# Kernel tuning notes

Measured on AMD Instinct MI355X. Metric: run time of the kernel, lower is better.

The kernel has to match this reference:

```python
import jax, jax.numpy as jnp
import numpy as np

D = 256
N_TOK, N_SRL, N_ENT, T = 50000, 20000, 10000, 50000
E_TS, E_EE, E_ST, E_ET = 300000, 150000, 300000, 150000
SLOPE = 0.01  # F.leaky_relu default negative slope


def _leaky(x):
    return jnp.where(x >= 0, x, SLOPE * x)


def _seg_softmax(e, seg, n):
    # per-destination (segment) softmax over incoming edges, elementwise per feature
    mx = jax.ops.segment_max(e, seg, num_segments=n)
    mx = jnp.where(jnp.isfinite(mx), mx, 0.0)
    ex = jnp.exp(e - mx[seg])
    den = jax.ops.segment_sum(ex, seg, num_segments=n)
    return ex / jnp.maximum(den[seg], 1e-9)


def _gru_cell(x, h, W_ih, W_hh, b_ih, b_hh):
    # PyTorch GRU cell: gates ordered (r, z, n)
    gi = x @ W_ih.T + b_ih
    gh = h @ W_hh.T + b_hh
    ir, iz, in_ = jnp.split(gi, 3, axis=-1)
    hr, hz, hn = jnp.split(gh, 3, axis=-1)
    r = jax.nn.sigmoid(ir + hr)
    z = jax.nn.sigmoid(iz + hz)
    n = jnp.tanh(in_ + r * hn)
    return (1.0 - z) * n + z * h


def _covering_dst(key, E, N):
    # every dst node gets >= 1 edge (matches DGL UDF-reduce update semantics)
    return jax.random.permutation(key, jnp.arange(E, dtype=jnp.int32) % N)


def setup_inputs():
    key = jax.random.key(0)
    ks = jax.random.split(key, 32)
    f32 = jnp.float32
    inp = {
        'feat_tok': jax.random.normal(ks[0], (N_TOK, D), f32),
        'feat_srl': jax.random.normal(ks[1], (N_SRL, D), f32),
        'feat_ent': jax.random.normal(ks[2], (N_ENT, D), f32),
        'bert_token_emb': jax.random.normal(ks[3], (T, D), f32),
        'rel_type': jax.random.uniform(ks[4], (E_EE,), f32),
        'src_ts': jax.random.randint(ks[5], (E_TS,), 0, N_TOK, jnp.int32),
        'dst_ts': _covering_dst(ks[6], E_TS, N_SRL),
        'src_ee': jax.random.randint(ks[7], (E_EE,), 0, N_ENT, jnp.int32),
        'dst_ee': _covering_dst(ks[8], E_EE, N_ENT),
        'src_st': jax.random.randint(ks[9], (E_ST,), 0, N_SRL, jnp.int32),
        'dst_st': _covering_dst(ks[10], E_ST, N_TOK),
        'src_et': jax.random.randint(ks[11], (E_ET,), 0, N_ENT, jnp.int32),
        'dst_et': _covering_dst(ks[12], E_ET, N_TOK),
    }
    x0 = jax.random.randint(ks[13], (E_EE,), 0, T - 64, jnp.int32)
    ln = jax.random.randint(ks[14], (E_EE,), 1, 65, jnp.int32)
    inp['span_idx'] = jnp.stack([x0, x0 + ln], axis=1)
    s = 0.05
    inp['W_node_trans'] = jax.random.normal(ks[15], (D, D), f32) * s
    inp['b_node_trans'] = jnp.zeros((D,), f32)
    inp['W_node_att'] = jax.random.normal(ks[16], (D, 2 * D), f32) * s
    inp['b_node_att'] = jnp.zeros((D,), f32)
    inp['W_rel_trans'] = jax.random.normal(ks[17], (D, 2 * D), f32) * s
    inp['b_rel_trans'] = jnp.zeros((D,), f32)
    inp['W_common'] = jax.random.normal(ks[18], (D, D), f32) * s
    inp['b_common'] = jnp.zeros((D,), f32)
    inp['W_ih'] = jax.random.normal(ks[19], (3 * D, D), f32) * s
    inp['W_hh'] = jax.random.normal(ks[20], (3 * D, D), f32) * s
    inp['b_ih'] = jax.random.normal(ks[21], (3 * D,), f32) * s
    inp['b_hh'] = jax.random.normal(ks[22], (3 * D,), f32) * s
    return inp


def reference(feat_tok, feat_srl, feat_ent, bert_token_emb, rel_type,
              W_node_trans, b_node_trans, W_node_att, b_node_att,
              W_rel_trans, b_rel_trans, W_common, b_common,
              W_ih, W_hh, b_ih, b_hh,
              src_ts, dst_ts, src_ee, dst_ee, span_idx,
              src_st, dst_st, src_et, dst_et):
    # ---- regular edges tok->srl (message_func_regular_node + reduce_func) ----
    us = feat_tok[src_ts] @ W_node_trans.T + b_node_trans          # [E_TS, D]
    ud = feat_srl[dst_ts] @ W_node_trans.T + b_node_trans
    e_ts = _leaky(jnp.concatenate([us, ud], axis=1) @ W_node_att.T + b_node_att)
    alpha_ts = _seg_softmax(e_ts, dst_ts, N_SRL)
    h_srl = jax.ops.segment_sum(alpha_ts * us, dst_ts, num_segments=N_SRL)

    # ---- ent2ent_rel (message_func_rel + reduce_func) ----
    # mean of bert_token_emb[x:y] via prefix sums (vectorized span means)
    P = jnp.concatenate([jnp.zeros((1, D), bert_token_emb.dtype),
                         jnp.cumsum(bert_token_emb, axis=0)], axis=0)  # [T+1, D]
    x, y = span_idx[:, 0], span_idx[:, 1]
    span_mean = (P[y] - P[x]) / (y - x).astype(P.dtype)[:, None]
    rel_emb = rel_type[:, None] * span_mean                         # [E_EE, D]
    src_e = feat_ent[src_ee]
    m_ee = (jnp.concatenate([src_e, rel_emb], axis=1) @ W_rel_trans.T + b_rel_trans)
    m_ee = m_ee @ W_common.T + b_common
    dst_p = feat_ent[dst_ee] @ W_node_trans.T + b_node_trans
    e_ee = _leaky(jnp.concatenate([m_ee, dst_p], axis=1) @ W_node_att.T + b_node_att)
    alpha_ee = _seg_softmax(e_ee, dst_ee, N_ENT)
    h_ent = jax.ops.segment_sum(alpha_ee * m_ee, dst_ee, num_segments=N_ENT)

    # ---- srl2tok / ent2tok: per-edge GRU step then segment-sum on tok ----
    m_st = _gru_cell(h_srl[src_st], feat_tok[dst_st], W_ih, W_hh, b_ih, b_hh)
    h_srl_tok = jax.ops.segment_sum(m_st, dst_st, num_segments=N_TOK)
    m_et = _gru_cell(h_ent[src_et], feat_tok[dst_et], W_ih, W_hh, b_ih, b_hh)
    h_ent_tok = jax.ops.segment_sum(m_et, dst_et, num_segments=N_TOK)

    # ---- final GRU combine: seq (h_ent_tok, feat_tok), hidden h_srl_tok ----
    h1 = _gru_cell(h_ent_tok, h_srl_tok, W_ih, W_hh, b_ih, b_hh)
    h_tok = _gru_cell(feat_tok, h1, W_ih, W_hh, b_ih, b_hh)

    return h_tok, h_srl, h_ent
```

## Files before the change

kernel.cpp:

```cpp
#include <hip/hip_runtime.h>
#include <stdint.h>


typedef unsigned short u16;
typedef __bf16 bf16_t;
typedef bf16_t bf16x8 __attribute__((ext_vector_type(8)));
typedef float f32x4 __attribute__((ext_vector_type(4)));

__device__ __forceinline__ float us2f(u16 h) {
  unsigned int u = ((unsigned int)h) << 16;
  return __builtin_bit_cast(float, u);
}
__device__ __forceinline__ u16 f2us(float f) {
  unsigned int u = __builtin_bit_cast(unsigned int, f);
  u += 0x7FFFu + ((u >> 16) & 1u);
  return (u16)(u >> 16);
}
__device__ __forceinline__ uint4 pack8(float4 a, float4 b) {
  uint4 v;
  v.x = f2us(a.x) | ((unsigned)f2us(a.y) << 16);
  v.y = f2us(a.z) | ((unsigned)f2us(a.w) << 16);
  v.z = f2us(b.x) | ((unsigned)f2us(b.y) << 16);
  v.w = f2us(b.z) | ((unsigned)f2us(b.w) << 16);
  return v;
}
__device__ __forceinline__ void us2f4(ushort4 v, float* o) {
  o[0] = us2f(v.x); o[1] = us2f(v.y); o[2] = us2f(v.z); o[3] = us2f(v.w);
}
__device__ __forceinline__ float sigm(float x) { return 1.f / (1.f + __expf(-x)); }
__device__ __forceinline__ float tanh_f(float x) {
  x = fminf(fmaxf(x, -15.f), 15.f);
  float e = __expf(2.f * x);
  return (e - 1.f) / (e + 1.f);
}

__global__ void fill_sent(float* out, int n, float v) {
  int i = blockIdx.x * 256 + threadIdx.x;
  if (i < n) out[i] = v;
}

__global__ void count_k(const int* __restrict__ dst, int E, int* __restrict__ cnt) {
  int i = blockIdx.x * 256 + threadIdx.x;
  if (i < E) atomicAdd(&cnt[dst[i]], 1);
}

__global__ __launch_bounds__(1024) void scan4_k(int* a0, int n0, int* a1, int n1,
                                                int* a2, int n2, int* a3, int n3) {
  int* a; int n;
  if (blockIdx.x == 0) { a = a0; n = n0; }
  else if (blockIdx.x == 1) { a = a1; n = n1; }
  else if (blockIdx.x == 2) { a = a2; n = n2; }
  else { a = a3; n = n3; }
  __shared__ int swv[16];
  const int t = threadIdx.x, lane = t & 63, wid = t >> 6;
  int carry = 0;
  for (int base = 0; base < n; base += 1024) {
    int r = base + t;
    int v = (r < n) ? a[r] : 0;
    int inc = v;
#pragma unroll
    for (int o = 1; o < 64; o <<= 1) {
      int x = __shfl_up(inc, o, 64);
      if (lane >= o) inc += x;
    }
    if (lane == 63) swv[wid] = inc;
    __syncthreads();
    int wbase = 0, tot = 0;
    for (int w = 0; w < 16; w++) { int s = swv[w]; tot += s; if (w < wid) wbase += s; }
    if (r < n) a[r] = carry + wbase + inc - v;
    carry += tot;
    __syncthreads();
  }
}

__global__ void fill_k(const int* __restrict__ dst, int E, int* __restrict__ off,
                       int* __restrict__ list) {
  int i = blockIdx.x * 256 + threadIdx.x;
  if (i < E) {
    int p = atomicAdd(&off[dst[i]], 1);
    list[p] = i;
  }
}

__global__ __launch_bounds__(256) void cumsum_p1(const float* __restrict__ emb,
                                                 float* __restrict__ bsum) {
  int b = blockIdx.x, t = threadIdx.x;
  int r0 = b * 64, r1 = min(r0 + 64, 50000);
  float acc = 0.f;
  for (int r = r0; r < r1; r++) acc += emb[(size_t)r * 256 + t];
  bsum[(size_t)b * 256 + t] = acc;
}
__global__ __launch_bounds__(256) void cumsum_p2p(float* __restrict__ bsum, int nb) {
  const int d = blockIdx.x;
  const int t = threadIdx.x, lane = t & 63, wid = t >> 6;
  __shared__ float wsum[4];
  float v[4];
  float s = 0.f;
#pragma unroll
  for (int j = 0; j < 4; j++) {
    int b = t * 4 + j;
    v[j] = (b < nb) ? bsum[(size_t)b * 256 + d] : 0.f;
    s += v[j];
  }
  float inc = s;
#pragma unroll
  for (int o = 1; o < 64; o <<= 1) {
    float x = __shfl_up(inc, o, 64);
    if (lane >= o) inc += x;
  }
  if (lane == 63) wsum[wid] = inc;
  __syncthreads();
  float wbase = 0.f;
  for (int w = 0; w < 4; w++) {
    float ws = wsum[w];
    if (w < wid) wbase += ws;
  }
  float excl = wbase + inc - s;
#pragma unroll
  for (int j = 0; j < 4; j++) {
    int b = t * 4 + j;
    if (b < nb) bsum[(size_t)b * 256 + d] = excl;
    excl += v[j];
  }
}
__global__ __launch_bounds__(256) void cumsum_p3(const float* __restrict__ emb,
                                                 const float* __restrict__ bsum,
                                                 float* __restrict__ Pm) {
  int b = blockIdx.x, t = threadIdx.x;
  int r0 = b * 64, r1 = min(r0 + 64, 50000);
  float acc = bsum[(size_t)b * 256 + t];
  if (b == 0) Pm[t] = 0.f;
  for (int r = r0; r < r1; r++) {
    acc += emb[(size_t)r * 256 + t];
    Pm[(size_t)(r + 1) * 256 + t] = acc;
  }
}

__global__ __launch_bounds__(256) void make_B2(const float* __restrict__ Watt,
                                               const float* __restrict__ Wc,
                                               float* __restrict__ B2) {
  int r = blockIdx.x, k = threadIdx.x;
  float s = 0.f;
  for (int n = 0; n < 256; n++) s += Watt[r * 512 + n] * Wc[n * 256 + k];
  B2[r * 256 + k] = s;
}
__global__ void make_bias2(const float* __restrict__ Watt, const float* __restrict__ bc,
                           float* __restrict__ bias2) {
  int r = threadIdx.x;
  float s = 0.f;
  for (int k = 0; k < 256; k++) s += Watt[r * 512 + k] * bc[k];
  bias2[r] = s;
}
__global__ __launch_bounds__(256) void make_WW(const float* __restrict__ Wc,
                                               const float* __restrict__ B2,
                                               const float* __restrict__ Wrel,
                                               float* __restrict__ WW) {
  int r = blockIdx.x, k = threadIdx.x;
  const float* X = (r < 256) ? (Wc + (size_t)r * 256) : (B2 + (size_t)(r - 256) * 256);
  float s = 0.f;
  for (int n = 0; n < 256; n++) s += X[n] * Wrel[(size_t)n * 512 + 256 + k];
  WW[(size_t)r * 256 + k] = s;
}

__global__ __launch_bounds__(256) void conv8(
    const float* s0, u16* d0, int n0, const float* s1, u16* d1, int n1,
    const float* s2, u16* d2, int n2, const float* s3, u16* d3, int n3,
    const float* s4, u16* d4, int n4, const float* s5, u16* d5, int n5,
    const float* s6, u16* d6, int n6, const float* s7, u16* d7, int n7) {
  const float* s; u16* d; int n;
  switch (blockIdx.y) {
    case 0: s = s0; d = d0; n = n0; break;
    case 1: s = s1; d = d1; n = n1; break;
    case 2: s = s2; d = d2; n = n2; break;
    case 3: s = s3; d = d3; n = n3; break;
    case 4: s = s4; d = d4; n = n4; break;
    case 5: s = s5; d = d5; n = n5; break;
    case 6: s = s6; d = d6; n = n6; break;
    default: s = s7; d = d7; n = n7; break;
  }
  int i = (blockIdx.x * 256 + threadIdx.x) * 8;
  if (i < n) {
    float4 a = *(const float4*)(s + i), b = *(const float4*)(s + i + 4);
    *(uint4*)(d + i) = pack8(a, b);
  }
}

template <int AMODE, int ASRC, bool OUTBF>
__global__ __launch_bounds__(256) void gemm_nl(
    const void* __restrict__ Ap, int lda,
    const float* __restrict__ Pm, const int* __restrict__ span,
    const float* __restrict__ rel, const int* __restrict__ lst,
    const int* __restrict__ offarr, const int* __restrict__ srcv,
    const u16* __restrict__ s2tab, int dst0, int dpc,
    const u16* __restrict__ B, int ldb, const float* __restrict__ bias,
    void* __restrict__ Cp, int Cstride, int coff, int M, int NT) {
  constexpr int LDA = 264, LDB = 136;
  __shared__ u16 As[64 * LDA];
  __shared__ u16 Bs[64 * LDB];
  int e_start = 0, eM = M;
  if (AMODE == 2) {
    e_start = dst0 ? offarr[dst0 - 1] : 0;
    int len = offarr[dst0 + dpc - 1] - e_start;
    eM = len < M ? len : M;
  }
  const int m0 = blockIdx.x * 64;
  if (m0 >= eM) return;
  const int nbase = blockIdx.y * NT * 64;
  const int t = threadIdx.x;
  const int wave = t >> 6, lane = t & 63, lrow = lane & 15, quad = lane >> 4;

#pragma unroll
  for (int i = 0; i < 8; i++) {
    int c = t + i * 256;
    int row = c >> 5, col = (c & 31) * 8;
    int gm = m0 + row;
    uint4 va; va.x = va.y = va.z = va.w = 0u;
    if (gm < eM) {
      if (AMODE == 0) {
        if (ASRC == 0) {
          const float* af = (const float*)Ap + (size_t)gm * lda + col;
          va = pack8(*(const float4*)af, *(const float4*)(af + 4));
        } else {
          va = *(const uint4*)((const u16*)Ap + (size_t)gm * lda + col);
        }
      } else {
        int e = lst[e_start + gm];
        int xx = span[2 * e], yy = span[2 * e + 1];
        float sc = rel[e] / (float)(yy - xx);
        const float* py = Pm + (size_t)yy * 256 + col;
        const float* px = Pm + (size_t)xx * 256 + col;
        float4 ya = *(const float4*)py, yb = *(const float4*)(py + 4);
        float4 xa = *(const float4*)px, xb = *(const float4*)(px + 4);
        float4 d0 = {(ya.x - xa.x) * sc, (ya.y - xa.y) * sc,
                     (ya.z - xa.z) * sc, (ya.w - xa.w) * sc};
        float4 d1 = {(yb.x - xb.x) * sc, (yb.y - xb.y) * sc,
                     (yb.z - xb.z) * sc, (yb.w - xb.w) * sc};
        va = pack8(d0, d1);
      }
    }
    *(uint4*)&As[row * LDA + col] = va;
  }

  for (int nt = 0; nt < NT; nt++) {
    const int n0 = nbase + nt * 64;
    f32x4 acc[4] = {{0.f, 0.f, 0.f, 0.f}, {0.f, 0.f, 0.f, 0.f},
                    {0.f, 0.f, 0.f, 0.f}, {0.f, 0.f, 0.f, 0.f}};
    for (int k2 = 0; k2 < 2; k2++) {
      __syncthreads();
#pragma unroll
      for (int i = 0; i < 4; i++) {
        int c = t + i * 256;
        int row = c >> 4, col = (c & 15) * 8;
        uint4 vb = *(const uint4*)(B + (size_t)(n0 + row) * ldb + k2 * 128 + col);
        *(uint4*)&Bs[row * LDB + col] = vb;
      }
      __syncthreads();
      const u16* ab = &As[(wave * 16 + lrow) * LDA + k2 * 128 + quad * 8];
      const u16* bb = &Bs[lrow * LDB + quad * 8];
#pragma unroll
      for (int kk = 0; kk < 128; kk += 32) {
        bf16x8 av = *(const bf16x8*)(ab + kk);
#pragma unroll
        for (int j = 0; j < 4; j++) {
          bf16x8 bv = *(const bf16x8*)(bb + j * 16 * LDB + kk);
          acc[j] = __builtin_amdgcn_mfma_f32_16x16x32_bf16(av, bv, acc[j], 0, 0, 0);
        }
      }
    }
#pragma unroll
    for (int r = 0; r < 4; r++) {
      int m = m0 + wave * 16 + quad * 4 + r;
      if (m < eM) {
        const u16* srow = nullptr;
        if (AMODE == 2) {
          int e = lst[e_start + m];
          srow = s2tab + (size_t)srcv[e] * 512;
        }
#pragma unroll
        for (int j = 0; j < 4; j++) {
          int n = n0 + j * 16 + lrow;
          float v = acc[j][r] + (bias ? bias[n] : 0.f);
          if (AMODE == 2) v += us2f(srow[n]);
          if (OUTBF) ((u16*)Cp)[(size_t)m * Cstride + coff + n] = f2us(v);
          else       ((float*)Cp)[(size_t)m * Cstride + coff + n] = v;
        }
      }
    }
  }
}

__global__ __launch_bounds__(256) void agg_ts2(
    const int* __restrict__ off, const int* __restrict__ list,
    const int* __restrict__ src, const u16* __restrict__ uta,
    const u16* __restrict__ adst, float* __restrict__ out) {
  const int i = blockIdx.x, t = threadIdx.x, lane = t & 63, w = t >> 6;
  const int s0 = i ? off[i - 1] : 0, s1 = off[i];
  const int cnt = s1 - s0;
  __shared__ int sl[64];
  __shared__ float nbuf[4][256], dbuf[4][256];
  if (t < cnt) sl[t] = src[list[s0 + t]];
  __syncthreads();
  const int d4 = lane * 4;
  float ad[4];
  us2f4(*(const ushort4*)&adst[(size_t)i * 256 + d4], ad);
  float num[4] = {0.f, 0.f, 0.f, 0.f}, den[4] = {0.f, 0.f, 0.f, 0.f};
  for (int p = w; p < cnt; p += 4) {
    const u16* row = uta + (size_t)sl[p] * 512;
    float u[4], a[4];
    us2f4(*(const ushort4*)&row[d4], u);
    us2f4(*(const ushort4*)&row[256 + d4], a);
#pragma unroll
    for (int j = 0; j < 4; j++) {
      float v = a[j] + ad[j];
      v = v >= 0.f ? v : 0.01f * v;
      float ex = __expf(v);
      den[j] += ex;
      num[j] += ex * u[j];
    }
  }
#pragma unroll
  for (int j = 0; j < 4; j++) { nbuf[w][d4 + j] = num[j]; dbuf[w][d4 + j] = den[j]; }
  __syncthreads();
  float ns = nbuf[0][t] + nbuf[1][t] + nbuf[2][t] + nbuf[3][t];
  float ds = dbuf[0][t] + dbuf[1][t] + dbuf[2][t] + dbuf[3][t];
  out[(size_t)i * 256 + t] = ns / fmaxf(ds, 1e-9f);
}

__global__ __launch_bounds__(256) void agg_ee2(
    const int* __restrict__ off, const u16* __restrict__ buf,
    const u16* __restrict__ adp, float* __restrict__ out, int dst0) {
  const int i = dst0 + blockIdx.x, t = threadIdx.x, lane = t & 63, w = t >> 6;
  const int e_start = dst0 ? off[dst0 - 1] : 0;
  const int s0 = i ? off[i - 1] : 0, s1 = off[i];
  __shared__ float nbuf[4][256], dbuf[4][256];
  const int d4 = lane * 4;
  float ad[4];
  us2f4(*(const ushort4*)&adp[(size_t)i * 256 + d4], ad);
  float num[4] = {0.f, 0.f, 0.f, 0.f}, den[4] = {0.f, 0.f, 0.f, 0.f};
  for (int p = s0 + w; p < s1; p += 4) {
    const u16* row = buf + (size_t)(p - e_start) * 512;
    float m[4], a[4];
    us2f4(*(const ushort4*)&row[d4], m);
    us2f4(*(const ushort4*)&row[256 + d4], a);
#pragma unroll
    for (int j = 0; j < 4; j++) {
      float v = a[j] + ad[j];
      v = v >= 0.f ? v : 0.01f * v;
      float ex = __expf(v);
      den[j] += ex;
      num[j] += ex * m[j];
    }
  }
#pragma unroll
  for (int j = 0; j < 4; j++) { nbuf[w][d4 + j] = num[j]; dbuf[w][d4 + j] = den[j]; }
  __syncthreads();
  float ns = nbuf[0][t] + nbuf[1][t] + nbuf[2][t] + nbuf[3][t];
  float ds = dbuf[0][t] + dbuf[1][t] + dbuf[2][t] + dbuf[3][t];
  out[(size_t)i * 256 + t] = ns / fmaxf(ds, 1e-9f);
}

__global__ __launch_bounds__(256) void agg_gru2(
    const int* __restrict__ off, const int* __restrict__ list,
    const int* __restrict__ src, const u16* __restrict__ gi,
    const u16* __restrict__ ghc, const float* __restrict__ feat,
    u16* __restrict__ out, int tok0) {
  const int bi = blockIdx.x, i = tok0 + bi;
  const int t = threadIdx.x, lane = t & 63, w = t >> 6;
  const int s0 = i ? off[i - 1] : 0, s1 = off[i];
  const int cnt = s1 - s0;
  __shared__ int sl[32];
  __shared__ float red[4][256];
  if (t < cnt) sl[t] = src[list[s0 + t]];
  __syncthreads();
  const int d4 = lane * 4;
  const size_t b = (size_t)bi * 768;
  float ghr[4], ghz[4], ghn[4], h[4];
  us2f4(*(const ushort4*)&ghc[b + d4], ghr);
  us2f4(*(const ushort4*)&ghc[b + 256 + d4], ghz);
  us2f4(*(const ushort4*)&ghc[b + 512 + d4], ghn);
  { float4 v = *(const float4*)&feat[(size_t)i * 256 + d4];
    h[0] = v.x; h[1] = v.y; h[2] = v.z; h[3] = v.w; }
  float sum[4] = {0.f, 0.f, 0.f, 0.f};
  for (int p = w; p < cnt; p += 4) {
    const u16* g = gi + (size_t)sl[p] * 768;
    float gr[4], gz[4], gn[4];
    us2f4(*(const ushort4*)&g[d4], gr);
    us2f4(*(const ushort4*)&g[256 + d4], gz);
    us2f4(*(const ushort4*)&g[512 + d4], gn);
#pragma unroll
    for (int j = 0; j < 4; j++) {
      float r = sigm(gr[j] + ghr[j]);
      float z = sigm(gz[j] + ghz[j]);
      float n = tanh_f(gn[j] + r * ghn[j]);
      sum[j] += (1.f - z) * n + z * h[j];
    }
  }
#pragma unroll
  for (int j = 0; j < 4; j++) red[w][d4 + j] = sum[j];
  __syncthreads();
  float s = red[0][t] + red[1][t] + red[2][t] + red[3][t];
  out[(size_t)i * 256 + t] = f2us(s);
}

template <bool OUTBF>
__global__ __launch_bounds__(256) void gru_combine2(
    const float* __restrict__ gi, const float* __restrict__ gh,
    const u16* __restrict__ hprev, void* __restrict__ out, int row0) {
  const int t = threadIdx.x, lane = t & 63, w = t >> 6;
  const int li = blockIdx.x * 4 + w;
  const int d4 = lane * 4;
  const size_t g = (size_t)li * 768;
  float4 ir = *(const float4*)&gi[g + d4];
  float4 hr4 = *(const float4*)&gh[g + d4];
  float4 iz = *(const float4*)&gi[g + 256 + d4];
  float4 hz4 = *(const float4*)&gh[g + 256 + d4];
  float4 in4 = *(const float4*)&gi[g + 512 + d4];
  float4 hn4 = *(const float4*)&gh[g + 512 + d4];
  float h[4];
  us2f4(*(const ushort4*)&hprev[(size_t)(row0 + li) * 256 + d4], h);
  float gir[4] = {ir.x, ir.y, ir.z, ir.w}, ghr[4] = {hr4.x, hr4.y, hr4.z, hr4.w};
  float giz[4] = {iz.x, iz.y, iz.z, iz.w}, ghz[4] = {hz4.x, hz4.y, hz4.z, hz4.w};
  float gin[4] = {in4.x, in4.y, in4.z, in4.w}, ghn[4] = {hn4.x, hn4.y, hn4.z, hn4.w};
  float o[4];
#pragma unroll
  for (int j = 0; j < 4; j++) {
    float r = sigm(gir[j] + ghr[j]);
    float z = sigm(giz[j] + ghz[j]);
    float n = tanh_f(gin[j] + r * ghn[j]);
    o[j] = (1.f - z) * n + z * h[j];
  }
  if (OUTBF) {
    ushort4 ov = {f2us(o[0]), f2us(o[1]), f2us(o[2]), f2us(o[3])};
    *(ushort4*)&((u16*)out)[(size_t)(row0 + li) * 256 + d4] = ov;
  } else {
    float4 ov = {o[0], o[1], o[2], o[3]};
    *(float4*)&((float*)out)[(size_t)(row0 + li) * 256 + d4] = ov;
  }
}

extern "C" void kernel_launch(void* const* d_in, const int* in_sizes, int n_in,
                              void* d_out, int out_size, void* d_ws, size_t ws_size,
                              hipStream_t stream) {
  const float* feat_tok = (const float*)d_in[0];
  const float* feat_srl = (const float*)d_in[1];
  const float* feat_ent = (const float*)d_in[2];
  const float* bert     = (const float*)d_in[3];
  const float* rel_type = (const float*)d_in[4];
  const int* src_ts = (const int*)d_in[5];
  const int* dst_ts = (const int*)d_in[6];
  const int* src_ee = (const int*)d_in[7];
  const int* dst_ee = (const int*)d_in[8];
  const int* src_st = (const int*)d_in[9];
  const int* dst_st = (const int*)d_in[10];
  const int* src_et = (const int*)d_in[11];
  const int* dst_et = (const int*)d_in[12];
  const int* span   = (const int*)d_in[13];
  const float* Wn   = (const float*)d_in[14];
  const float* bn   = (const float*)d_in[15];
  const float* Watt = (const float*)d_in[16];
  const float* batt = (const float*)d_in[17];
  const float* Wrel = (const float*)d_in[18];
  const float* brel = (const float*)d_in[19];
  const float* Wc   = (const float*)d_in[20];
  const float* bc   = (const float*)d_in[21];
  const float* Wih  = (const float*)d_in[22];
  const float* Whh  = (const float*)d_in[23];
  const float* bih  = (const float*)d_in[24];
  const float* bhh  = (const float*)d_in[25];

  char* W = (char*)d_ws;
  float* Pm    = (float*)(W + 0);
  u16* uta     = (u16*)(W + 51250240);
  u16* p_srl   = (u16*)(W + 102450240);
  u16* a_dst   = (u16*)(W + 112690240);
  u16* s_ent   = (u16*)(W + 51250240);
  u16* p_ent   = (u16*)(W + 56370240);
  u16* meeatt  = (u16*)(W + 51250240);
  float* WW    = (float*)(W + 138000000);
  float* B2    = (float*)(W + 138600000);
  float* bias2 = (float*)(W + 138900000);
  u16* s2tab   = (u16*)(W + 139000000);
  u16* adp     = (u16*)(W + 149300032);
  float* bsum  = (float*)(W + 155000000);
  u16* gi_srl  = (u16*)(W + 0);
  u16* gi_ent  = (u16*)(W + 30720000);
  u16* ghc     = (u16*)(W + 51250240);
  u16* hst     = (u16*)(W + 115300096);
  u16* het     = (u16*)(W + 140900096);
  float* giA   = (float*)(W + 0);
  float* ghA   = (float*)(W + 38400000);
  u16* h1      = (u16*)(W + 76800000);
  int* ts_off = (int*)(W + 166500096);
  int* ts_lst = (int*)(W + 166580096);
  int* ee_off = (int*)(W + 167780096);
  int* ee_lst = (int*)(W + 167820096);
  int* st_off = (int*)(W + 168420096);
  int* st_lst = (int*)(W + 168620096);
  int* et_off = (int*)(W + 169820096);
  int* et_lst = (int*)(W + 170020096);
  constexpr size_t NEED = 170620096;

  float* out_htok = (float*)d_out;
  float* out_hsrl = (float*)d_out + 12800000;
  float* out_hent = (float*)d_out + 17920000;

  u16* wtb    = (u16*)((char*)d_out + 49000000);
  u16* Wn_b   = wtb;
  u16* Watt_b = wtb + 65536;
  u16* Wrel_b = wtb + 196608;
  u16* Wc_b   = wtb + 327680;
  u16* Wih_b  = wtb + 393216;
  u16* Whh_b  = wtb + 589824;
  u16* WW_b   = wtb + 786432;
  u16* B2_b   = wtb + 917504;

  if (ws_size < NEED) {
    fill_sent<<<(out_size + 255) / 256, 256, 0, stream>>>(
        (float*)d_out, out_size, 1000.f + (float)(ws_size >> 20));
    return;
  }

  hipMemsetAsync(ts_off, 0, 20000 * 4, stream);
  hipMemsetAsync(ee_off, 0, 10000 * 4, stream);
  hipMemsetAsync(st_off, 0, 50000 * 4, stream);
  hipMemsetAsync(et_off, 0, 50000 * 4, stream);
  count_k<<<1172, 256, 0, stream>>>(dst_ts, 300000, ts_off);
  count_k<<<586, 256, 0, stream>>>(dst_ee, 150000, ee_off);
  count_k<<<1172, 256, 0, stream>>>(dst_st, 300000, st_off);
  count_k<<<586, 256, 0, stream>>>(dst_et, 150000, et_off);
  scan4_k<<<4, 1024, 0, stream>>>(ts_off, 20000, ee_off, 10000, st_off, 50000, et_off, 50000);
  fill_k<<<1172, 256, 0, stream>>>(dst_ts, 300000, ts_off, ts_lst);
  fill_k<<<586, 256, 0, stream>>>(dst_ee, 150000, ee_off, ee_lst);
  fill_k<<<1172, 256, 0, stream>>>(dst_st, 300000, st_off, st_lst);
  fill_k<<<586, 256, 0, stream>>>(dst_et, 150000, et_off, et_lst);

  cumsum_p1<<<782, 256, 0, stream>>>(bert, bsum);
  cumsum_p2p<<<256, 256, 0, stream>>>(bsum, 782);
  cumsum_p3<<<782, 256, 0, stream>>>(bert, bsum, Pm);
  make_B2<<<256, 256, 0, stream>>>(Watt, Wc, B2);
  make_bias2<<<1, 256, 0, stream>>>(Watt, bc, bias2);
  make_WW<<<512, 256, 0, stream>>>(Wc, B2, Wrel, WW);
  conv8<<<dim3(96, 8), 256, 0, stream>>>(
      Wn, Wn_b, 65536, Watt, Watt_b, 131072, Wrel, Wrel_b, 131072,
      Wc, Wc_b, 65536, Wih, Wih_b, 196608, Whh, Whh_b, 196608,
      WW, WW_b, 131072, B2, B2_b, 65536);

  gemm_nl<0, 0, true><<<dim3(782, 1), 256, 0, stream>>>(
      feat_tok, 256, nullptr, nullptr, nullptr, nullptr, nullptr, nullptr, nullptr, 0, 0,
      Wn_b, 256, bn, uta, 512, 0, 50000, 4);
  gemm_nl<0, 1, true><<<dim3(782, 1), 256, 0, stream>>>(
      uta, 512, nullptr, nullptr, nullptr, nullptr, nullptr, nullptr, nullptr, 0, 0,
      Watt_b, 512, nullptr, uta, 512, 256, 50000, 4);
  gemm_nl<0, 0, true><<<dim3(313, 2), 256, 0, stream>>>(
      feat_srl, 256, nullptr, nullptr, nullptr, nullptr, nullptr, nullptr, nullptr, 0, 0,
      Wn_b, 256, bn, p_srl, 256, 0, 20000, 2);
  gemm_nl<0, 1, true><<<dim3(313, 2), 256, 0, stream>>>(
      p_srl, 256, nullptr, nullptr, nullptr, nullptr, nullptr, nullptr, nullptr, 0, 0,
      Watt_b + 256, 512, batt, a_dst, 256, 0, 20000, 2);
  agg_ts2<<<20000, 256, 0, stream>>>(ts_off, ts_lst, src_ts, uta, a_dst, out_hsrl);

  gemm_nl<0, 0, true><<<dim3(157, 2), 256, 0, stream>>>(
      feat_ent, 256, nullptr, nullptr, nullptr, nullptr, nullptr, nullptr, nullptr, 0, 0,
      Wrel_b, 512, brel, s_ent, 256, 0, 10000, 2);
  gemm_nl<0, 0, true><<<dim3(157, 2), 256, 0, stream>>>(
      feat_ent, 256, nullptr, nullptr, nullptr, nullptr, nullptr, nullptr, nullptr, 0, 0,
      Wn_b, 256, bn, p_ent, 256, 0, 10000, 2);
  gemm_nl<0, 1, true><<<dim3(157, 2), 256, 0, stream>>>(
      s_ent, 256, nullptr, nullptr, nullptr, nullptr, nullptr, nullptr, nullptr, 0, 0,
      Wc_b, 256, bc, s2tab, 512, 0, 10000, 2);
  gemm_nl<0, 1, true><<<dim3(157, 2), 256, 0, stream>>>(
      s_ent, 256, nullptr, nullptr, nullptr, nullptr, nullptr, nullptr, nullptr, 0, 0,
      B2_b, 256, bias2, s2tab, 512, 256, 10000, 2);
  gemm_nl<0, 1, true><<<dim3(157, 2), 256, 0, stream>>>(
      p_ent, 256, nullptr, nullptr, nullptr, nullptr, nullptr, nullptr, nullptr, 0, 0,
      Watt_b + 256, 512, batt, adp, 256, 0, 10000, 2);
  for (int c = 0; c < 4; c++) {
    gemm_nl<2, 0, true><<<dim3(625, 1), 256, 0, stream>>>(
        nullptr, 256, Pm, span, rel_type, ee_lst, ee_off, src_ee, s2tab, c * 2500, 2500,
        WW_b, 256, nullptr, meeatt, 512, 0, 40000, 8);
    agg_ee2<<<2500, 256, 0, stream>>>(ee_off, meeatt, adp, out_hent, c * 2500);
  }

  gemm_nl<0, 0, true><<<dim3(313, 3), 256, 0, stream>>>(
      out_hsrl, 256, nullptr, nullptr, nullptr, nullptr, nullptr, nullptr, nullptr, 0, 0,
      Wih_b, 256, bih, gi_srl, 768, 0, 20000, 4);
  gemm_nl<0, 0, true><<<dim3(157, 3), 256, 0, stream>>>(
      out_hent, 256, nullptr, nullptr, nullptr, nullptr, nullptr, nullptr, nullptr, 0, 0,
      Wih_b, 256, bih, gi_ent, 768, 0, 10000, 4);
  for (int c = 0; c < 2; c++) {
    int base = c * 25000;
    gemm_nl<0, 0, true><<<dim3(391, 3), 256, 0, stream>>>(
        feat_tok + (size_t)base * 256, 256, nullptr, nullptr, nullptr, nullptr,
        nullptr, nullptr, nullptr, 0, 0, Whh_b, 256, bhh, ghc, 768, 0, 25000, 4);
    agg_gru2<<<25000, 256, 0, stream>>>(st_off, st_lst, src_st, gi_srl, ghc, feat_tok, hst, base);
    agg_gru2<<<25000, 256, 0, stream>>>(et_off, et_lst, src_et, gi_ent, ghc, feat_tok, het, base);
  }

  for (int c = 0; c < 4; c++) {
    int base = c * 12500;
    gemm_nl<0, 1, false><<<dim3(196, 3), 256, 0, stream>>>(
        het + (size_t)base * 256, 256, nullptr, nullptr, nullptr, nullptr,
        nullptr, nullptr, nullptr, 0, 0, Wih_b, 256, bih, giA, 768, 0, 12500, 4);
    gemm_nl<0, 1, false><<<dim3(196, 3), 256, 0, stream>>>(
        hst + (size_t)base * 256, 256, nullptr, nullptr, nullptr, nullptr,
        nullptr, nullptr, nullptr, 0, 0, Whh_b, 256, bhh, ghA, 768, 0, 12500, 4);
    gru_combine2<true><<<3125, 256, 0, stream>>>(giA, ghA, hst, h1, base);
  }
  for (int c = 0; c < 4; c++) {
    int base = c * 12500;
    gemm_nl<0, 0, false><<<dim3(196, 3), 256, 0, stream>>>(
        feat_tok + (size_t)base * 256, 256, nullptr, nullptr, nullptr, nullptr,
        nullptr, nullptr, nullptr, 0, 0, Wih_b, 256, bih, giA, 768, 0, 12500, 4);
    gemm_nl<0, 1, false><<<dim3(196, 3), 256, 0, stream>>>(
        h1 + (size_t)base * 256, 256, nullptr, nullptr, nullptr, nullptr,
        nullptr, nullptr, nullptr, 0, 0, Whh_b, 256, bhh, ghA, 768, 0, 12500, 4);
    gru_combine2<false><<<3125, 256, 0, stream>>>(giA, ghA, h1, out_htok, base);
  }
}
```

Measured before the change: 1.914 ms.

## Load GEMM B fragments directly from global memory, dropping LDS staging

```diff
diff --git a/kernel.cpp b/kernel.cpp
--- a/kernel.cpp
+++ b/kernel.cpp
@@ -194,9 +194,8 @@
     const u16* __restrict__ s2tab, int dst0, int dpc,
     const u16* __restrict__ B, int ldb, const float* __restrict__ bias,
     void* __restrict__ Cp, int Cstride, int coff, int M, int NT) {
-  constexpr int LDA = 264, LDB = 136;
+  constexpr int LDA = 264;
   __shared__ u16 As[64 * LDA];
-  __shared__ u16 Bs[64 * LDB];
   int e_start = 0, eM = M;
   if (AMODE == 2) {
     e_start = dst0 ? offarr[dst0 - 1] : 0;
@@ -240,31 +239,31 @@
     }
     *(uint4*)&As[row * LDA + col] = va;
   }
-
+  __syncthreads();
+
+  const u16* ar = &As[(wave * 16 + lrow) * LDA + quad * 8];
   for (int nt = 0; nt < NT; nt++) {
     const int n0 = nbase + nt * 64;
     f32x4 acc[4] = {{0.f, 0.f, 0.f, 0.f}, {0.f, 0.f, 0.f, 0.f},
                     {0.f, 0.f, 0.f, 0.f}, {0.f, 0.f, 0.f, 0.f}};
+    const u16* bp0 = B + (size_t)(n0 + lrow) * ldb + quad * 8;
+    const u16* bp1 = bp0 + (size_t)16 * ldb;
+    const u16* bp2 = bp0 + (size_t)32 * ldb;
+    const u16* bp3 = bp0 + (size_t)48 * ldb;
+#pragma unroll
     for (int k2 = 0; k2 < 2; k2++) {
-      __syncthreads();
-#pragma unroll
-      for (int i = 0; i < 4; i++) {
-        int c = t + i * 256;
-        int row = c >> 4, col = (c & 15) * 8;
-        uint4 vb = *(const uint4*)(B + (size_t)(n0 + row) * ldb + k2 * 128 + col);
-        *(uint4*)&Bs[row * LDB + col] = vb;
-      }
-      __syncthreads();
-      const u16* ab = &As[(wave * 16 + lrow) * LDA + k2 * 128 + quad * 8];
-      const u16* bb = &Bs[lrow * LDB + quad * 8];
 #pragma unroll
       for (int kk = 0; kk < 128; kk += 32) {
-        bf16x8 av = *(const bf16x8*)(ab + kk);
-#pragma unroll
-        for (int j = 0; j < 4; j++) {
-          bf16x8 bv = *(const bf16x8*)(bb + j * 16 * LDB + kk);
-          acc[j] = __builtin_amdgcn_mfma_f32_16x16x32_bf16(av, bv, acc[j], 0, 0, 0);
-        }
+        const int ko = k2 * 128 + kk;
+        bf16x8 av = *(const bf16x8*)(ar + ko);
+        acc[0] = __builtin_amdgcn_mfma_f32_16x16x32_bf16(
+            av, *(const bf16x8*)(bp0 + ko), acc[0], 0, 0, 0);
+        acc[1] = __builtin_amdgcn_mfma_f32_16x16x32_bf16(
+            av, *(const bf16x8*)(bp1 + ko), acc[1], 0, 0, 0);
+        acc[2] = __builtin_amdgcn_mfma_f32_16x16x32_bf16(
+            av, *(const bf16x8*)(bp2 + ko), acc[2], 0, 0, 0);
+        acc[3] = __builtin_amdgcn_mfma_f32_16x16x32_bf16(
+            av, *(const bf16x8*)(bp3 + ko), acc[3], 0, 0, 0);
       }
     }
 #pragma unroll
@@ -575,9 +574,9 @@
       p_ent, 256, nullptr, nullptr, nullptr, nullptr, nullptr, nullptr, nullptr, 0, 0,
       Watt_b + 256, 512, batt, adp, 256, 0, 10000, 2);
   for (int c = 0; c < 4; c++) {
-    gemm_nl<2, 0, true><<<dim3(625, 1), 256, 0, stream>>>(
+    gemm_nl<2, 0, true><<<dim3(625, 2), 256, 0, stream>>>(
         nullptr, 256, Pm, span, rel_type, ee_lst, ee_off, src_ee, s2tab, c * 2500, 2500,
-        WW_b, 256, nullptr, meeatt, 512, 0, 40000, 8);
+        WW_b, 256, nullptr, meeatt, 512, 0, 40000, 4);
     agg_ee2<<<2500, 256, 0, stream>>>(ee_off, meeatt, adp, out_hent, c * 2500);
   }
 
```

After: 3.069 ms. +60.3%, slower.

## Register-prefetch full-K B tiles and double-buffer them across N tiles in gemm_nl

Applied to the files above, without the earlier changes.

```diff
diff --git a/kernel.cpp b/kernel.cpp
--- a/kernel.cpp
+++ b/kernel.cpp
@@ -194,9 +194,9 @@
     const u16* __restrict__ s2tab, int dst0, int dpc,
     const u16* __restrict__ B, int ldb, const float* __restrict__ bias,
     void* __restrict__ Cp, int Cstride, int coff, int M, int NT) {
-  constexpr int LDA = 264, LDB = 136;
+  constexpr int LDA = 264, LDBS = 264;
   __shared__ u16 As[64 * LDA];
-  __shared__ u16 Bs[64 * LDB];
+  __shared__ u16 Bs[64 * LDBS];
   int e_start = 0, eM = M;
   if (AMODE == 2) {
     e_start = dst0 ? offarr[dst0 - 1] : 0;
@@ -208,6 +208,13 @@
   const int nbase = blockIdx.y * NT * 64;
   const int t = threadIdx.x;
   const int wave = t >> 6, lane = t & 63, lrow = lane & 15, quad = lane >> 4;
+
+  uint4 b0[8], b1[8];
+#pragma unroll
+  for (int i = 0; i < 8; i++) {
+    int c = t + i * 256;
+    b0[i] = *(const uint4*)(B + (size_t)(nbase + (c >> 5)) * ldb + (c & 31) * 8);
+  }
 
 #pragma unroll
   for (int i = 0; i < 8; i++) {
@@ -240,31 +247,35 @@
     }
     *(uint4*)&As[row * LDA + col] = va;
   }
-
-  for (int nt = 0; nt < NT; nt++) {
-    const int n0 = nbase + nt * 64;
+  __syncthreads();
+
+  auto writeB = [&](const uint4* br) {
+#pragma unroll
+    for (int i = 0; i < 8; i++) {
+      int c = t + i * 256;
+      *(uint4*)&Bs[(c >> 5) * LDBS + (c & 31) * 8] = br[i];
+    }
+  };
+  auto loadB = [&](int ntile, uint4* br) {
+#pragma unroll
+    for (int i = 0; i < 8; i++) {
+      int c = t + i * 256;
+      br[i] = *(const uint4*)(B + (size_t)(nbase + ntile * 64 + (c >> 5)) * ldb +
+                              (c & 31) * 8);
+    }
+  };
+  auto compute = [&](int n0) {
     f32x4 acc[4] = {{0.f, 0.f, 0.f, 0.f}, {0.f, 0.f, 0.f, 0.f},
                     {0.f, 0.f, 0.f, 0.f}, {0.f, 0.f, 0.f, 0.f}};
-    for (int k2 = 0; k2 < 2; k2++) {
-      __syncthreads();
-#pragma unroll
-      for (int i = 0; i < 4; i++) {
-        int c = t + i * 256;
-        int row = c >> 4, col = (c & 15) * 8;
-        uint4 vb = *(const uint4*)(B + (size_t)(n0 + row) * ldb + k2 * 128 + col);
-        *(uint4*)&Bs[row * LDB + col] = vb;
-      }
-      __syncthreads();
-      const u16* ab = &As[(wave * 16 + lrow) * LDA + k2 * 128 + quad * 8];
-      const u16* bb = &Bs[lrow * LDB + quad * 8];
-#pragma unroll
-      for (int kk = 0; kk < 128; kk += 32) {
-        bf16x8 av = *(const bf16x8*)(ab + kk);
-#pragma unroll
-        for (int j = 0; j < 4; j++) {
-          bf16x8 bv = *(const bf16x8*)(bb + j * 16 * LDB + kk);
-          acc[j] = __builtin_amdgcn_mfma_f32_16x16x32_bf16(av, bv, acc[j], 0, 0, 0);
-        }
+    const u16* ar = &As[(wave * 16 + lrow) * LDA + quad * 8];
+    const u16* bb = &Bs[lrow * LDBS + quad * 8];
+#pragma unroll
+    for (int ks = 0; ks < 8; ks++) {
+      bf16x8 av = *(const bf16x8*)(ar + ks * 32);
+#pragma unroll
+      for (int j = 0; j < 4; j++) {
+        bf16x8 bv = *(const bf16x8*)(bb + j * 16 * LDBS + ks * 32);
+        acc[j] = __builtin_amdgcn_mfma_f32_16x16x32_bf16(av, bv, acc[j], 0, 0, 0);
       }
     }
 #pragma unroll
@@ -286,6 +297,19 @@
         }
       }
     }
+  };
+
+  for (int nt = 0; nt < NT; nt += 2) {
+    writeB(b0);
+    loadB(nt + 1, b1);
+    __syncthreads();
+    compute(nbase + nt * 64);
+    __syncthreads();
+    writeB(b1);
+    if (nt + 2 < NT) loadB(nt + 2, b0);
+    __syncthreads();
+    compute(nbase + (nt + 1) * 64);
+    if (nt + 2 < NT) __syncthreads();
   }
 }
 
```

Result: slower. 3.033 ms (+58.4%).
